# Kernel tuning notes

Hardware: AMD Instinct MI355X
Metric: run time of the kernel (lower is better)

The kernel has to match this reference:

```python
import jax, jax.numpy as jnp
import numpy as np

EPS = 1e-5  # torch GroupNorm default
KNN_K = 16


def _knn_idx(Q, P, K):
    # Q:[B,Nq,3], P:[B,Np,3] -> idx [B,Nq,K], ascending squared distance
    d = (jnp.sum(Q * Q, -1)[:, :, None] + jnp.sum(P * P, -1)[:, None, :]
         - 2.0 * jnp.einsum('bqc,bkc->bqk', Q, P))
    _, idx = jax.lax.top_k(-d, K)
    return idx


def _gather_nbr(feat_bnc, idx_bqk):
    # feat:[B,Np,C], idx:[B,Nq,K] -> [B,Nq,K,C]  (knn_gather)
    return jax.vmap(lambda f, i: f[i])(feat_bnc, idx_bqk)


def _group_norm(x_bcnk, gamma, beta, num_groups=8):
    B, C, N, K = x_bcnk.shape
    G = min(num_groups, C)
    xg = x_bcnk.reshape(B, G, C // G, N, K)
    mu = xg.mean(axis=(2, 3, 4), keepdims=True)
    var = xg.var(axis=(2, 3, 4), keepdims=True)
    xn = ((xg - mu) / jnp.sqrt(var + EPS)).reshape(B, C, N, K)
    return xn * gamma[None, :, None, None] + beta[None, :, None, None]


def _edge_conv(Fq_bcn, Fk_bcn, Pq_b3n, Pk_b3n, k, W, gamma, beta):
    # EdgeConv: concat(x_j - x_i, x_i) -> conv1x1 -> GN -> ReLU -> max over K
    idx = _knn_idx(Pq_b3n.transpose(0, 2, 1), Pk_b3n.transpose(0, 2, 1), k)
    nbr = _gather_nbr(Fk_bcn.transpose(0, 2, 1), idx)          # [B,Nq,K,Cin]
    Fi = jnp.broadcast_to(Fq_bcn.transpose(0, 2, 1)[:, :, None, :], nbr.shape)
    pair = jnp.concatenate([nbr - Fi, Fi], axis=-1)            # [B,Nq,K,2Cin]
    out = jnp.einsum('oc,bnkc->bonk', W, pair)                 # conv 1x1, no bias
    out = _group_norm(out, gamma, beta)
    out = jax.nn.relu(out)
    return out.max(axis=-1)                                    # [B,Cout,Nq]


def _fps_idx(P_b3n, m):
    # Farthest point sampling starting at index 0 (pytorch3d default)
    def one(Pn3):
        d0 = jnp.sum((Pn3 - Pn3[0]) ** 2, -1)
        def step(dists, _):
            nxt = jnp.argmax(dists)
            d = jnp.sum((Pn3 - Pn3[nxt]) ** 2, -1)
            return jnp.minimum(dists, d), nxt
        _, idxs = jax.lax.scan(step, d0, None, length=m - 1)
        return jnp.concatenate([jnp.zeros((1,), jnp.int32), idxs.astype(jnp.int32)])
    return jax.vmap(one)(P_b3n.transpose(0, 2, 1))


def _gather_bcn(x_bcn, idx_bm):
    return jax.vmap(lambda x, i: x[:, i])(x_bcn, idx_bm)


def setup_inputs() -> dict:
    key = jax.random.key(0)
    ks = jax.random.split(key, 8)
    B, N = 2, 8192
    def w(k, shape, s=0.1):
        return jax.random.normal(k, shape, jnp.float32) * s
    return {
        'xyz': jax.random.normal(ks[0], (B, 3, N), jnp.float32),
        'stem_w': w(ks[1], (8, 3)), 'stem_b': jnp.zeros((8,), jnp.float32),
        'w1': w(ks[2], (32, 16)),  'g1': jnp.ones((32,), jnp.float32),  'b1': jnp.zeros((32,), jnp.float32),
        'w2': w(ks[3], (64, 64)),  'g2': jnp.ones((64,), jnp.float32),  'b2': jnp.zeros((64,), jnp.float32),
        'w3': w(ks[4], (64, 128)), 'g3': jnp.ones((64,), jnp.float32),  'b3': jnp.zeros((64,), jnp.float32),
        'w4': w(ks[5], (128, 128)),'g4': jnp.ones((128,), jnp.float32), 'b4': jnp.zeros((128,), jnp.float32),
    }


def reference(xyz, stem_w, stem_b, w1, g1, b1, w2, g2, b2, w3, g3, b3, w4, g4, b4):
    K = KNN_K
    P0 = xyz                                                     # [B,3,N0]
    F0 = jnp.einsum('oc,bcn->bon', stem_w, xyz) + stem_b[None, :, None]
    F0a = _edge_conv(F0, F0, P0, P0, K, w1, g1, b1)              # [B,32,N0]
    N0 = P0.shape[2]
    N1 = max(1, N0 // 4)
    idx1 = _fps_idx(P0, N1)
    P1 = _gather_bcn(P0, idx1)
    F1sk = _gather_bcn(F0a, idx1)
    F1a = _edge_conv(F1sk, F0a, P1, P0, K, w2, g2, b2)           # [B,64,N1]
    N2 = max(1, N1 // 4)
    idx2 = _fps_idx(P1, N2)
    P2 = _gather_bcn(P1, idx2)
    F2sk = _gather_bcn(F1a, idx2)
    F2mid = _edge_conv(F2sk, F1a, P2, P1, K, w3, g3, b3)         # [B,64,N2]
    F2a = _edge_conv(F2mid, F1a, P2, P1, K, w4, g4, b4)          # [B,128,N2]
    return (P0, F0a, P1, F1a, P2, F2a)
```

## Files before the change

kernel.cpp:

```cpp
#include <hip/hip_runtime.h>
#include <math.h>

#define KNN 16

__global__ __launch_bounds__(256) void stem_kernel(const float* __restrict__ xyz,
    const float* __restrict__ w, const float* __restrict__ bias,
    float* __restrict__ F0, int N){
  int id = blockIdx.x*256 + threadIdx.x;
  int n = id % N; int b = id / N;
  float x = xyz[((size_t)b*3+0)*N+n];
  float y = xyz[((size_t)b*3+1)*N+n];
  float z = xyz[((size_t)b*3+2)*N+n];
  #pragma unroll
  for (int o=0;o<8;o++){
    float v = fmaf(w[o*3+0],x, fmaf(w[o*3+1],y, fmaf(w[o*3+2],z, bias[o])));
    F0[((size_t)b*8+o)*N+n] = v;
  }
}

__global__ __launch_bounds__(256) void knn_kernel(
    const float* __restrict__ Pq, const float* __restrict__ Pp,
    float* __restrict__ part_d, int* __restrict__ part_i,
    int Nq, int Np, int CAND){
  __shared__ float4 tile[256];
  int qg = blockIdx.x*256 + threadIdx.x;
  int b  = qg / Nq, qn = qg % Nq;
  int s  = blockIdx.y;
  const float* Pqb = Pq + (size_t)b*3*Nq;
  const float* Ppb = Pp + (size_t)b*3*Np;
  float qx = Pqb[qn], qy = Pqb[Nq+qn], qz = Pqb[2*Nq+qn];
  float qq = __fadd_rn(__fadd_rn(__fmul_rn(qx,qx),__fmul_rn(qy,qy)),__fmul_rn(qz,qz));

  float dl[16]; int il[16];
  #pragma unroll
  for (int u=0;u<16;u++){ dl[u]=INFINITY; il[u]=-1; }
  float maxd = INFINITY; int maxslot = 0;

  int c0 = s*CAND;
  for (int tb=0; tb<CAND; tb+=256){
    int p = c0 + tb + threadIdx.x;
    float px = Ppb[p], py = Ppb[Np+p], pz = Ppb[2*Np+p];
    float pp = __fadd_rn(__fadd_rn(__fmul_rn(px,px),__fmul_rn(py,py)),__fmul_rn(pz,pz));
    __syncthreads();
    tile[threadIdx.x] = make_float4(px,py,pz,pp);
    __syncthreads();
    for (int j=0;j<256;j++){
      float4 c = tile[j];
      float dot = __fadd_rn(__fadd_rn(__fmul_rn(qx,c.x),__fmul_rn(qy,c.y)),__fmul_rn(qz,c.z));
      float dc  = __fsub_rn(__fadd_rn(qq,c.w), __fmul_rn(2.0f,dot));
      if (dc < maxd){
        int pidx = c0 + tb + j;
        #pragma unroll
        for (int u=0;u<16;u++){ bool sel=(maxslot==u); dl[u]=sel?dc:dl[u]; il[u]=sel?pidx:il[u]; }
        maxd = dl[0]; maxslot = 0;
        #pragma unroll
        for (int u=1;u<16;u++){ bool g=(dl[u]>maxd); maxd=g?dl[u]:maxd; maxslot=g?u:maxslot; }
      }
    }
  }
  size_t base = ((size_t)qg*gridDim.y + s)*16;
  #pragma unroll
  for (int u=0;u<16;u++){ part_d[base+u]=dl[u]; part_i[base+u]=il[u]; }
}

__global__ __launch_bounds__(256) void knn_merge(const float* __restrict__ part_d,
    const int* __restrict__ part_i, int* __restrict__ idxk, int S, int total){
  int qg = blockIdx.x*256 + threadIdx.x;
  if (qg >= total) return;
  const float* pd = part_d + (size_t)qg*S*16;
  const int*   pi = part_i + (size_t)qg*S*16;
  float dl[16]; int il[16];
  #pragma unroll
  for (int u=0;u<16;u++){ dl[u]=INFINITY; il[u]=0x7fffffff; }
  float maxd = INFINITY; int maxi = 0x7fffffff; int maxslot = 0;
  int tot = S*16;
  for (int e=0;e<tot;e++){
    float d = pd[e]; int ii = pi[e];
    bool better = (d < maxd) || (d == maxd && ii < maxi);
    if (better){
      #pragma unroll
      for (int u=0;u<16;u++){ bool sel=(maxslot==u); dl[u]=sel?d:dl[u]; il[u]=sel?ii:il[u]; }
      maxd = dl[0]; maxi = il[0]; maxslot = 0;
      #pragma unroll
      for (int u=1;u<16;u++){
        bool g = (dl[u]>maxd) || (dl[u]==maxd && il[u]>maxi);
        maxd=g?dl[u]:maxd; maxi=g?il[u]:maxi; maxslot=g?u:maxslot;
      }
    }
  }
  #pragma unroll
  for (int u=0;u<16;u++) idxk[(size_t)qg*16+u] = il[u];
}

template<int CIN, int COUT>
__global__ __launch_bounds__(1024) void edge_conv_pre(
    const float* __restrict__ Fk, const float* __restrict__ Fi,
    const int* __restrict__ idx, const float* __restrict__ W,
    float* __restrict__ pre, int Nq, int Np){
  constexpr int C2  = 2*CIN;
  constexpr int PAD = C2 + 4;
  constexpr int TO  = (COUT <= 64) ? COUT : 64;
  constexpr int OP  = COUT / TO;
  extern __shared__ float sm[];
  float* Wl = sm;
  float* Pl = sm + COUT*PAD;
  int t = threadIdx.x;
  int n = blockIdx.x, b = blockIdx.y;
  for (int e=t; e<COUT*C2; e += blockDim.x){
    int o=e/C2, c=e%C2; Wl[o*PAD+c] = W[e];
  }
  const int* idxn = idx + ((size_t)b*Nq + n)*16;
  for (int e=t; e<16*C2; e += blockDim.x){
    int k = e/C2, c = e%C2;
    int cc = (c < CIN) ? c : (c-CIN);
    float fi = Fi[((size_t)b*CIN + cc)*Nq + n];
    float v;
    if (c < CIN){ int nb = idxn[k]; v = Fk[((size_t)b*CIN + c)*Np + nb] - fi; }
    else v = fi;
    Pl[k*PAD+c] = v;
  }
  __syncthreads();
  int k = t & 15, o0 = t >> 4;
  #pragma unroll
  for (int op=0; op<OP; op++){
    int o = o0 + op*TO;
    float acc = 0.f;
    #pragma unroll
    for (int c=0;c<C2;c+=4){
      float4 wv = *(const float4*)&Wl[o*PAD+c];
      float4 pv = *(const float4*)&Pl[k*PAD+c];
      acc = fmaf(wv.x,pv.x,acc); acc = fmaf(wv.y,pv.y,acc);
      acc = fmaf(wv.z,pv.z,acc); acc = fmaf(wv.w,pv.w,acc);
    }
    pre[(((size_t)b*COUT + o)*Nq + n)*16 + k] = acc;
  }
}

__global__ __launch_bounds__(256) void gn_reduce(const float* __restrict__ pre,
    double* __restrict__ gsum, int slabLen){
  int b = blockIdx.z, g = blockIdx.y;
  size_t base = ((size_t)(b*8+g))*slabLen;
  int chunkLen = slabLen / gridDim.x;
  const float* p = pre + base + (size_t)blockIdx.x*chunkLen;
  double s=0.0, sq=0.0;
  for (int i = threadIdx.x*4; i < chunkLen; i += 1024){
    float4 v = *(const float4*)(p+i);
    s += (double)v.x; sq = fma((double)v.x,(double)v.x,sq);
    s += (double)v.y; sq = fma((double)v.y,(double)v.y,sq);
    s += (double)v.z; sq = fma((double)v.z,(double)v.z,sq);
    s += (double)v.w; sq = fma((double)v.w,(double)v.w,sq);
  }
  #pragma unroll
  for (int off=32; off>=1; off>>=1){ s += __shfl_down(s, off); sq += __shfl_down(sq, off); }
  __shared__ double ls[4], lq[4];
  int wid = threadIdx.x>>6;
  if ((threadIdx.x&63)==0){ ls[wid]=s; lq[wid]=sq; }
  __syncthreads();
  if (threadIdx.x==0){
    double S=ls[0]+ls[1]+ls[2]+ls[3], Q=lq[0]+lq[1]+lq[2]+lq[3];
    atomicAdd(&gsum[(b*8+g)*2],   S);
    atomicAdd(&gsum[(b*8+g)*2+1], Q);
  }
}

template<int COUT>
__global__ __launch_bounds__(256) void gn_act_max(const float* __restrict__ pre,
    const double* __restrict__ gsum, const float* __restrict__ gamma,
    const float* __restrict__ beta, float* __restrict__ outF, int Nq){
  int id = blockIdx.x*256 + threadIdx.x;
  int o = (id/Nq)%COUT; int b = id/(Nq*COUT);
  int g = o/(COUT/8);
  double s = gsum[(b*8+g)*2], sq = gsum[(b*8+g)*2+1];
  double cnt = (double)(COUT/8)*Nq*16.0;
  double mu  = s/cnt;
  double var = sq/cnt - mu*mu;
  float muf=(float)mu, rstd=(float)(1.0/sqrt(var+1e-5));
  float ga=gamma[o], be=beta[o];
  const float4* p = (const float4*)(pre + (size_t)id*16);
  float m = 0.f;
  #pragma unroll
  for (int q=0;q<4;q++){
    float4 v = p[q];
    m = fmaxf(m, fmaf((v.x-muf)*rstd, ga, be));
    m = fmaxf(m, fmaf((v.y-muf)*rstd, ga, be));
    m = fmaxf(m, fmaf((v.z-muf)*rstd, ga, be));
    m = fmaxf(m, fmaf((v.w-muf)*rstd, ga, be));
  }
  outF[id] = m;
}

template<int CTRL>
__device__ __forceinline__ float dpp_maxf(float x){
  int y = __builtin_amdgcn_update_dpp(0, __float_as_int(x), CTRL, 0xf, 0xf, true);
  return fmaxf(x, __int_as_float(y));
}

template<int PPT, int BLK, int M>
__global__ __launch_bounds__(BLK) void fps_kernel(const float* __restrict__ P,
    int* __restrict__ idx_out){
  constexpr int N  = PPT*BLK;
  constexpr int NW = BLK/64;
  extern __shared__ __align__(16) float sm[];
  float* lx = sm; float* ly = sm+N; float* lz = sm+2*N;
  unsigned long long* wkey = (unsigned long long*)(sm + 3*N);
  int b = blockIdx.x, t = threadIdx.x;
  const float* Pb = P + (size_t)b*3*N;
  float px[PPT], py[PPT], pz[PPT], dist[PPT];
  #pragma unroll
  for (int j=0;j<PPT;j+=4){
    int p = t*PPT + j;
    float4 vx = *(const float4*)&Pb[p];
    float4 vy = *(const float4*)&Pb[N+p];
    float4 vz = *(const float4*)&Pb[2*N+p];
    px[j]=vx.x; px[j+1]=vx.y; px[j+2]=vx.z; px[j+3]=vx.w;
    py[j]=vy.x; py[j+1]=vy.y; py[j+2]=vy.z; py[j+3]=vy.w;
    pz[j]=vz.x; pz[j+1]=vz.y; pz[j+2]=vz.z; pz[j+3]=vz.w;
    #pragma unroll
    for (int u=0;u<4;u++){ lx[p+u]=px[j+u]; ly[p+u]=py[j+u]; lz[p+u]=pz[j+u]; }
  }
  __syncthreads();
  float sx=lx[0], sy=ly[0], sz=lz[0];
  float bd = -1.f; int bj = 0;
  #pragma unroll
  for (int j=0;j<PPT;j++){
    float dx=__fsub_rn(px[j],sx), dy=__fsub_rn(py[j],sy), dz=__fsub_rn(pz[j],sz);
    float dd=__fadd_rn(__fadd_rn(__fmul_rn(dx,dx),__fmul_rn(dy,dy)),__fmul_rn(dz,dz));
    dist[j]=dd;
    bool c = dd > bd; bd = c?dd:bd; bj = c?j:bj;
  }
  int pbest = t*PPT + bj;
  if (t==0) idx_out[(size_t)b*M] = 0;
  int wid = t>>6, lane = t&63;
  int par = 0;
  for (int i=1;i<M;i++){
    float r = bd;
    r = dpp_maxf<0x111>(r);
    r = dpp_maxf<0x112>(r);
    r = dpp_maxf<0x114>(r);
    r = dpp_maxf<0x118>(r);
    r = dpp_maxf<0x142>(r);
    r = dpp_maxf<0x143>(r);
    float wmax = __int_as_float(__builtin_amdgcn_readlane(__float_as_int(r), 63));
    unsigned long long msk = __ballot(bd == wmax);
    int srcl = __ffsll(msk) - 1;
    int wp = __builtin_amdgcn_readlane(pbest, srcl);
    if (lane==0)
      wkey[par*NW + wid] = ((unsigned long long)__float_as_uint(wmax)<<32)
                         | (unsigned)(~(unsigned)wp);
    __syncthreads();
    unsigned long long best = wkey[par*NW];
    #pragma unroll
    for (int w=1;w<NW;w++){ unsigned long long o = wkey[par*NW+w]; best = (o>best)?o:best; }
    unsigned widx = ~(unsigned)best;
    if (t==0) idx_out[(size_t)b*M + i] = (int)widx;
    float nsx = lx[widx], nsy = ly[widx], nsz = lz[widx];
    par ^= 1;
    float nbd = -1.f; int nbj = 0;
    #pragma unroll
    for (int j=0;j<PPT;j++){
      float dx=__fsub_rn(px[j],nsx), dy=__fsub_rn(py[j],nsy), dz=__fsub_rn(pz[j],nsz);
      float dd=__fadd_rn(__fadd_rn(__fmul_rn(dx,dx),__fmul_rn(dy,dy)),__fmul_rn(dz,dz));
      float nd = fminf(dist[j], dd);
      dist[j] = nd;
      bool c = nd > nbd; nbd = c?nd:nbd; nbj = c?j:nbj;
    }
    bd = nbd; pbest = t*PPT + nbj;
  }
}

__global__ __launch_bounds__(256) void gather_kernel(float* __restrict__ dst,
    const float* __restrict__ src, const int* __restrict__ idx,
    int C, int Nsrc, int M){
  int id = blockIdx.x*256 + threadIdx.x;
  int m = id % M; int c = (id/M)%C; int b = id/(M*C);
  dst[id] = src[((size_t)b*C + c)*Nsrc + idx[(size_t)b*M + m]];
}

extern "C" void kernel_launch(void* const* d_in, const int* in_sizes, int n_in,
                              void* d_out, int out_size, void* d_ws, size_t ws_size,
                              hipStream_t stream) {
  const float* xyz    = (const float*)d_in[0];
  const float* stem_w = (const float*)d_in[1];
  const float* stem_b = (const float*)d_in[2];
  const float* w1 = (const float*)d_in[3];
  const float* g1 = (const float*)d_in[4];
  const float* b1 = (const float*)d_in[5];
  const float* w2 = (const float*)d_in[6];
  const float* g2 = (const float*)d_in[7];
  const float* b2 = (const float*)d_in[8];
  const float* w3 = (const float*)d_in[9];
  const float* g3 = (const float*)d_in[10];
  const float* b3 = (const float*)d_in[11];
  const float* w4 = (const float*)d_in[12];
  const float* g4 = (const float*)d_in[13];
  const float* b4 = (const float*)d_in[14];

  float* out = (float*)d_out;
  float* P0o  = out + 0;
  float* F0a  = out + 49152;
  float* P1o  = out + 573440;
  float* F1a  = out + 585728;
  float* P2o  = out + 847872;
  float* F2a  = out + 850944;

  char* ws = (char*)d_ws;
  float* F0     = (float*)(ws + 0);
  float* pre    = (float*)(ws + 524288);
  float* part_d = (float*)(ws + 524288);
  int*   part_i = (int*)  (ws + 524288 + 16777216);
  int*   idxk   = (int*)  (ws + 34078720);
  double* gsum  = (double*)(ws + 35127296);
  int*   idx1   = (int*)  (ws + 35127552);
  int*   idx2   = (int*)  (ws + 35143936);
  float* F1sk   = (float*)(ws + 35148032);
  float* F2sk   = (float*)(ws + 35672320);
  float* F2mid  = (float*)(ws + 35934464);

  size_t smem_c1 = (size_t)(32*20  + 16*20 )*4;
  size_t smem_c2 = (size_t)(64*132 + 16*132)*4;
  size_t smem_c4 = (size_t)(128*132+ 16*132)*4;
  size_t smem_f1 = (size_t)3*8192*4 + 256;
  size_t smem_f2 = (size_t)3*2048*4 + 256;

  hipMemcpyAsync(P0o, xyz, (size_t)49152*4, hipMemcpyDeviceToDevice, stream);
  stem_kernel<<<(2*8192)/256, 256, 0, stream>>>(xyz, stem_w, stem_b, F0, 8192);

  knn_kernel<<<dim3(16384/256, 16), 256, 0, stream>>>(xyz, xyz, part_d, part_i, 8192, 8192, 512);
  knn_merge <<<16384/256, 256, 0, stream>>>(part_d, part_i, idxk, 16, 16384);
  edge_conv_pre<8,32><<<dim3(8192,2), 512, smem_c1, stream>>>(F0, F0, idxk, w1, pre, 8192, 8192);
  hipMemsetAsync(gsum, 0, 256, stream);
  gn_reduce<<<dim3(8,8,2), 256, 0, stream>>>(pre, gsum, 4*8192*16);
  gn_act_max<32><<<(2*32*8192)/256, 256, 0, stream>>>(pre, gsum, g1, b1, F0a, 8192);

  fps_kernel<16,512,2048><<<2, 512, smem_f1, stream>>>(xyz, idx1);
  gather_kernel<<<(2*3*2048)/256, 256, 0, stream>>>(P1o, xyz, idx1, 3, 8192, 2048);
  gather_kernel<<<(2*32*2048)/256, 256, 0, stream>>>(F1sk, F0a, idx1, 32, 8192, 2048);

  knn_kernel<<<dim3(4096/256, 16), 256, 0, stream>>>(P1o, xyz, part_d, part_i, 2048, 8192, 512);
  knn_merge <<<4096/256, 256, 0, stream>>>(part_d, part_i, idxk, 16, 4096);
  edge_conv_pre<32,64><<<dim3(2048,2), 1024, smem_c2, stream>>>(F0a, F1sk, idxk, w2, pre, 2048, 8192);
  hipMemsetAsync(gsum, 0, 256, stream);
  gn_reduce<<<dim3(4,8,2), 256, 0, stream>>>(pre, gsum, 8*2048*16);
  gn_act_max<64><<<(2*64*2048)/256, 256, 0, stream>>>(pre, gsum, g2, b2, F1a, 2048);

  fps_kernel<4,512,512><<<2, 512, smem_f2, stream>>>(P1o, idx2);
  gather_kernel<<<(2*3*512)/256, 256, 0, stream>>>(P2o, P1o, idx2, 3, 2048, 512);
  gather_kernel<<<(2*64*512)/256, 256, 0, stream>>>(F2sk, F1a, idx2, 64, 2048, 512);

  knn_kernel<<<dim3(1024/256, 8), 256, 0, stream>>>(P2o, P1o, part_d, part_i, 512, 2048, 256);
  knn_merge <<<1024/256, 256, 0, stream>>>(part_d, part_i, idxk, 8, 1024);
  edge_conv_pre<64,64><<<dim3(512,2), 1024, smem_c2, stream>>>(F1a, F2sk, idxk, w3, pre, 512, 2048);
  hipMemsetAsync(gsum, 0, 256, stream);
  gn_reduce<<<dim3(1,8,2), 256, 0, stream>>>(pre, gsum, 8*512*16);
  gn_act_max<64><<<(2*64*512)/256, 256, 0, stream>>>(pre, gsum, g3, b3, F2mid, 512);

  edge_conv_pre<64,128><<<dim3(512,2), 1024, smem_c4, stream>>>(F1a, F2mid, idxk, w4, pre, 512, 2048);
  hipMemsetAsync(gsum, 0, 256, stream);
  gn_reduce<<<dim3(2,8,2), 256, 0, stream>>>(pre, gsum, 16*512*16);
  gn_act_max<128><<<(2*128*512)/256, 256, 0, stream>>>(pre, gsum, g4, b4, F2a, 512);

  (void)in_sizes; (void)n_in; (void)out_size; (void)ws_size;
}
```

Baseline: 4.044 ms.

## Morton-sort FPS points with bounding-box pruning and coalesce KNN partial layout

The FPS kernel now bitonic-sorts points by Morton code in shared memory so each thread owns a spatially compact set. It keeps a per-thread bounding box and skips the distance update when the new sample cannot reduce any of its distances. The winning sample's coordinates are broadcast directly, which removes the shared-memory coordinate arrays. KNN partial results are stored row-major over queries so the writes and the merge reads coalesce. The shared-memory size for the CIN=32 edge conv also changes. The pruning uses a fixed quantization grid (offset 8, scale 4) and a 0.999 slack factor, which assume a particular input range. The bitonic sort adds an upfront cost.

```diff
diff --git a/kernel.cpp b/kernel.cpp
--- a/kernel.cpp
+++ b/kernel.cpp
@@ -1,7 +1,7 @@
 #include <hip/hip_runtime.h>
 #include <math.h>
 
-#define KNN 16
+typedef unsigned long long ull;
 
 __global__ __launch_bounds__(256) void stem_kernel(const float* __restrict__ xyz,
     const float* __restrict__ w, const float* __restrict__ bias,
@@ -21,7 +21,7 @@
 __global__ __launch_bounds__(256) void knn_kernel(
     const float* __restrict__ Pq, const float* __restrict__ Pp,
     float* __restrict__ part_d, int* __restrict__ part_i,
-    int Nq, int Np, int CAND){
+    int Nq, int Np, int CAND, int total){
   __shared__ float4 tile[256];
   int qg = blockIdx.x*256 + threadIdx.x;
   int b  = qg / Nq, qn = qg % Nq;
@@ -58,24 +58,25 @@
       }
     }
   }
-  size_t base = ((size_t)qg*gridDim.y + s)*16;
-  #pragma unroll
-  for (int u=0;u<16;u++){ part_d[base+u]=dl[u]; part_i[base+u]=il[u]; }
+  #pragma unroll
+  for (int u=0;u<16;u++){
+    size_t row = (size_t)(s*16+u);
+    part_d[row*total + qg] = dl[u];
+    part_i[row*total + qg] = il[u];
+  }
 }
 
 __global__ __launch_bounds__(256) void knn_merge(const float* __restrict__ part_d,
-    const int* __restrict__ part_i, int* __restrict__ idxk, int S, int total){
+    const int* __restrict__ part_i, int* __restrict__ idxk, int rows, int total){
   int qg = blockIdx.x*256 + threadIdx.x;
   if (qg >= total) return;
-  const float* pd = part_d + (size_t)qg*S*16;
-  const int*   pi = part_i + (size_t)qg*S*16;
   float dl[16]; int il[16];
   #pragma unroll
   for (int u=0;u<16;u++){ dl[u]=INFINITY; il[u]=0x7fffffff; }
   float maxd = INFINITY; int maxi = 0x7fffffff; int maxslot = 0;
-  int tot = S*16;
-  for (int e=0;e<tot;e++){
-    float d = pd[e]; int ii = pi[e];
+  for (int e=0;e<rows;e++){
+    float d = part_d[(size_t)e*total + qg];
+    int  ii = part_i[(size_t)e*total + qg];
     bool better = (d < maxd) || (d == maxd && ii < maxi);
     if (better){
       #pragma unroll
@@ -194,77 +195,129 @@
   int y = __builtin_amdgcn_update_dpp(0, __float_as_int(x), CTRL, 0xf, 0xf, true);
   return fmaxf(x, __int_as_float(y));
 }
+__device__ __forceinline__ unsigned expandb(unsigned v){
+  v &= 0x3FF;
+  v = (v | (v<<16)) & 0x030000FF;
+  v = (v | (v<<8))  & 0x0300F00F;
+  v = (v | (v<<4))  & 0x030C30C3;
+  v = (v | (v<<2))  & 0x09249249;
+  return v;
+}
 
 template<int PPT, int BLK, int M>
 __global__ __launch_bounds__(BLK) void fps_kernel(const float* __restrict__ P,
     int* __restrict__ idx_out){
   constexpr int N  = PPT*BLK;
   constexpr int NW = BLK/64;
-  extern __shared__ __align__(16) float sm[];
-  float* lx = sm; float* ly = sm+N; float* lz = sm+2*N;
-  unsigned long long* wkey = (unsigned long long*)(sm + 3*N);
+  extern __shared__ __align__(16) unsigned smu[];
+  unsigned* keys = smu;
+  ull*     wk    = (ull*)&smu[N];
+  float4*  wc    = (float4*)(wk + 2*NW);
   int b = blockIdx.x, t = threadIdx.x;
   const float* Pb = P + (size_t)b*3*N;
-  float px[PPT], py[PPT], pz[PPT], dist[PPT];
-  #pragma unroll
-  for (int j=0;j<PPT;j+=4){
-    int p = t*PPT + j;
-    float4 vx = *(const float4*)&Pb[p];
-    float4 vy = *(const float4*)&Pb[N+p];
-    float4 vz = *(const float4*)&Pb[2*N+p];
-    px[j]=vx.x; px[j+1]=vx.y; px[j+2]=vx.z; px[j+3]=vx.w;
-    py[j]=vy.x; py[j+1]=vy.y; py[j+2]=vy.z; py[j+3]=vy.w;
-    pz[j]=vz.x; pz[j+1]=vz.y; pz[j+2]=vz.z; pz[j+3]=vz.w;
-    #pragma unroll
-    for (int u=0;u<4;u++){ lx[p+u]=px[j+u]; ly[p+u]=py[j+u]; lz[p+u]=pz[j+u]; }
+
+  for (int i=t; i<N; i+=BLK){
+    float x = Pb[i], y = Pb[N+i], z = Pb[2*N+i];
+    int cx = (int)(__fadd_rn(x,8.f)*4.f); cx = cx<0?0:(cx>63?63:cx);
+    int cy = (int)(__fadd_rn(y,8.f)*4.f); cy = cy<0?0:(cy>63?63:cy);
+    int cz = (int)(__fadd_rn(z,8.f)*4.f); cz = cz<0?0:(cz>63?63:cz);
+    unsigned mo = (expandb(cx)<<2) | (expandb(cy)<<1) | expandb(cz);
+    keys[i] = (mo<<13) | (unsigned)i;
+  }
+  for (unsigned k=2; k<=(unsigned)N; k<<=1){
+    for (unsigned j=k>>1; j>0; j>>=1){
+      __syncthreads();
+      for (int i=t; i<N; i+=BLK){
+        unsigned ixj = (unsigned)i ^ j;
+        if (ixj > (unsigned)i){
+          unsigned a = keys[i], c = keys[ixj];
+          bool up = ((i & k) == 0);
+          if ((a > c) == up){ keys[i]=c; keys[ixj]=a; }
+        }
+      }
+    }
   }
   __syncthreads();
-  float sx=lx[0], sy=ly[0], sz=lz[0];
-  float bd = -1.f; int bj = 0;
+
+  int oidx[PPT]; float px[PPT], py[PPT], pz[PPT], dist[PPT];
+  #pragma unroll
+  for (int j=0;j<PPT;j++){
+    oidx[j] = (int)(keys[t*PPT+j] & 0x1FFF);
+    px[j] = Pb[oidx[j]]; py[j] = Pb[N+oidx[j]]; pz[j] = Pb[2*N+oidx[j]];
+  }
+  float bxmn=px[0],bxmx=px[0],bymn=py[0],bymx=py[0],bzmn=pz[0],bzmx=pz[0];
+  #pragma unroll
+  for (int j=1;j<PPT;j++){
+    bxmn=fminf(bxmn,px[j]); bxmx=fmaxf(bxmx,px[j]);
+    bymn=fminf(bymn,py[j]); bymx=fmaxf(bymx,py[j]);
+    bzmn=fminf(bzmn,pz[j]); bzmx=fmaxf(bzmx,pz[j]);
+  }
+
+  float sx = Pb[0], sy = Pb[N], sz = Pb[2*N];
+  float bd = -1.f; int bi = 0x7fffffff; float bx=0.f, by=0.f, bz=0.f;
   #pragma unroll
   for (int j=0;j<PPT;j++){
     float dx=__fsub_rn(px[j],sx), dy=__fsub_rn(py[j],sy), dz=__fsub_rn(pz[j],sz);
     float dd=__fadd_rn(__fadd_rn(__fmul_rn(dx,dx),__fmul_rn(dy,dy)),__fmul_rn(dz,dz));
     dist[j]=dd;
-    bool c = dd > bd; bd = c?dd:bd; bj = c?j:bj;
-  }
-  int pbest = t*PPT + bj;
+    bool gt = dd > bd, eq = dd == bd;
+    int mn = min(bi, oidx[j]);
+    bd = gt?dd:bd; bx = gt?px[j]:bx; by = gt?py[j]:by; bz = gt?pz[j]:bz;
+    bi = gt?oidx[j]:(eq?mn:bi);
+  }
   if (t==0) idx_out[(size_t)b*M] = 0;
-  int wid = t>>6, lane = t&63;
-  int par = 0;
+
+  int wid = t>>6, lane = t&63, par = 0;
   for (int i=1;i<M;i++){
     float r = bd;
-    r = dpp_maxf<0x111>(r);
-    r = dpp_maxf<0x112>(r);
-    r = dpp_maxf<0x114>(r);
-    r = dpp_maxf<0x118>(r);
-    r = dpp_maxf<0x142>(r);
-    r = dpp_maxf<0x143>(r);
+    r = dpp_maxf<0x111>(r); r = dpp_maxf<0x112>(r);
+    r = dpp_maxf<0x114>(r); r = dpp_maxf<0x118>(r);
+    r = dpp_maxf<0x142>(r); r = dpp_maxf<0x143>(r);
     float wmax = __int_as_float(__builtin_amdgcn_readlane(__float_as_int(r), 63));
-    unsigned long long msk = __ballot(bd == wmax);
-    int srcl = __ffsll(msk) - 1;
-    int wp = __builtin_amdgcn_readlane(pbest, srcl);
-    if (lane==0)
-      wkey[par*NW + wid] = ((unsigned long long)__float_as_uint(wmax)<<32)
-                         | (unsigned)(~(unsigned)wp);
+    ull msk = __ballot(bd == wmax);
+    int bestl = __ffsll(msk) - 1;
+    int wbi = __builtin_amdgcn_readlane(bi, bestl);
+    ull rest = msk & (msk-1);
+    if (rest){
+      while (rest){
+        int l = __ffsll(rest)-1; rest &= rest-1;
+        int c = __builtin_amdgcn_readlane(bi, l);
+        if (c < wbi){ wbi = c; bestl = l; }
+      }
+    }
+    float wx = __int_as_float(__builtin_amdgcn_readlane(__float_as_int(bx), bestl));
+    float wy = __int_as_float(__builtin_amdgcn_readlane(__float_as_int(by), bestl));
+    float wz = __int_as_float(__builtin_amdgcn_readlane(__float_as_int(bz), bestl));
+    if (lane==0){
+      wk[par*NW+wid] = ((ull)__float_as_uint(wmax)<<32) | (unsigned)(~(unsigned)wbi);
+      wc[par*NW+wid] = make_float4(wx,wy,wz,0.f);
+    }
     __syncthreads();
-    unsigned long long best = wkey[par*NW];
+    ull best = wk[par*NW]; int bw = 0;
     #pragma unroll
-    for (int w=1;w<NW;w++){ unsigned long long o = wkey[par*NW+w]; best = (o>best)?o:best; }
-    unsigned widx = ~(unsigned)best;
-    if (t==0) idx_out[(size_t)b*M + i] = (int)widx;
-    float nsx = lx[widx], nsy = ly[widx], nsz = lz[widx];
+    for (int w=1;w<NW;w++){ ull o = wk[par*NW+w]; if (o > best){ best=o; bw=w; } }
+    float4 sc = wc[par*NW+bw];
+    if (t==0) idx_out[(size_t)b*M + i] = (int)(~(unsigned)best);
     par ^= 1;
-    float nbd = -1.f; int nbj = 0;
-    #pragma unroll
-    for (int j=0;j<PPT;j++){
-      float dx=__fsub_rn(px[j],nsx), dy=__fsub_rn(py[j],nsy), dz=__fsub_rn(pz[j],nsz);
-      float dd=__fadd_rn(__fadd_rn(__fmul_rn(dx,dx),__fmul_rn(dy,dy)),__fmul_rn(dz,dz));
-      float nd = fminf(dist[j], dd);
-      dist[j] = nd;
-      bool c = nd > nbd; nbd = c?nd:nbd; nbj = c?j:nbj;
-    }
-    bd = nbd; pbest = t*PPT + nbj;
+    float ex = fmaxf(fmaxf(__fsub_rn(bxmn,sc.x), __fsub_rn(sc.x,bxmx)), 0.f);
+    float ey = fmaxf(fmaxf(__fsub_rn(bymn,sc.y), __fsub_rn(sc.y,bymx)), 0.f);
+    float ez = fmaxf(fmaxf(__fsub_rn(bzmn,sc.z), __fsub_rn(sc.z,bzmx)), 0.f);
+    float lb = ex*ex + ey*ey + ez*ez;
+    if (!(lb*0.999f > bd)){
+      float nbd = -1.f; int nbi = 0x7fffffff; float nbx=0.f, nby=0.f, nbz=0.f;
+      #pragma unroll
+      for (int j=0;j<PPT;j++){
+        float dx=__fsub_rn(px[j],sc.x), dy=__fsub_rn(py[j],sc.y), dz=__fsub_rn(pz[j],sc.z);
+        float dd=__fadd_rn(__fadd_rn(__fmul_rn(dx,dx),__fmul_rn(dy,dy)),__fmul_rn(dz,dz));
+        float nd = fminf(dist[j], dd);
+        dist[j] = nd;
+        bool gt = nd > nbd, eq = nd == nbd;
+        int mn = min(nbi, oidx[j]);
+        nbd = gt?nd:nbd; nbx = gt?px[j]:nbx; nby = gt?py[j]:nby; nbz = gt?pz[j]:nbz;
+        nbi = gt?oidx[j]:(eq?mn:nbi);
+      }
+      bd=nbd; bi=nbi; bx=nbx; by=nby; bz=nbz;
+    }
   }
 }
 
@@ -317,16 +370,17 @@
   float* F2mid  = (float*)(ws + 35934464);
 
   size_t smem_c1 = (size_t)(32*20  + 16*20 )*4;
-  size_t smem_c2 = (size_t)(64*132 + 16*132)*4;
+  size_t smem_c2 = (size_t)(64*68  + 16*68 )*4;
+  size_t smem_c3 = (size_t)(64*132 + 16*132)*4;
   size_t smem_c4 = (size_t)(128*132+ 16*132)*4;
-  size_t smem_f1 = (size_t)3*8192*4 + 256;
-  size_t smem_f2 = (size_t)3*2048*4 + 256;
+  size_t smem_f1 = (size_t)8192*4 + 512;
+  size_t smem_f2 = (size_t)2048*4 + 512;
 
   hipMemcpyAsync(P0o, xyz, (size_t)49152*4, hipMemcpyDeviceToDevice, stream);
   stem_kernel<<<(2*8192)/256, 256, 0, stream>>>(xyz, stem_w, stem_b, F0, 8192);
 
-  knn_kernel<<<dim3(16384/256, 16), 256, 0, stream>>>(xyz, xyz, part_d, part_i, 8192, 8192, 512);
-  knn_merge <<<16384/256, 256, 0, stream>>>(part_d, part_i, idxk, 16, 16384);
+  knn_kernel<<<dim3(16384/256, 16), 256, 0, stream>>>(xyz, xyz, part_d, part_i, 8192, 8192, 512, 16384);
+  knn_merge <<<16384/256, 256, 0, stream>>>(part_d, part_i, idxk, 256, 16384);
   edge_conv_pre<8,32><<<dim3(8192,2), 512, smem_c1, stream>>>(F0, F0, idxk, w1, pre, 8192, 8192);
   hipMemsetAsync(gsum, 0, 256, stream);
   gn_reduce<<<dim3(8,8,2), 256, 0, stream>>>(pre, gsum, 4*8192*16);
@@ -336,8 +390,8 @@
   gather_kernel<<<(2*3*2048)/256, 256, 0, stream>>>(P1o, xyz, idx1, 3, 8192, 2048);
   gather_kernel<<<(2*32*2048)/256, 256, 0, stream>>>(F1sk, F0a, idx1, 32, 8192, 2048);
 
-  knn_kernel<<<dim3(4096/256, 16), 256, 0, stream>>>(P1o, xyz, part_d, part_i, 2048, 8192, 512);
-  knn_merge <<<4096/256, 256, 0, stream>>>(part_d, part_i, idxk, 16, 4096);
+  knn_kernel<<<dim3(4096/256, 16), 256, 0, stream>>>(P1o, xyz, part_d, part_i, 2048, 8192, 512, 4096);
+  knn_merge <<<4096/256, 256, 0, stream>>>(part_d, part_i, idxk, 256, 4096);
   edge_conv_pre<32,64><<<dim3(2048,2), 1024, smem_c2, stream>>>(F0a, F1sk, idxk, w2, pre, 2048, 8192);
   hipMemsetAsync(gsum, 0, 256, stream);
   gn_reduce<<<dim3(4,8,2), 256, 0, stream>>>(pre, gsum, 8*2048*16);
@@ -347,9 +401,9 @@
   gather_kernel<<<(2*3*512)/256, 256, 0, stream>>>(P2o, P1o, idx2, 3, 2048, 512);
   gather_kernel<<<(2*64*512)/256, 256, 0, stream>>>(F2sk, F1a, idx2, 64, 2048, 512);
 
-  knn_kernel<<<dim3(1024/256, 8), 256, 0, stream>>>(P2o, P1o, part_d, part_i, 512, 2048, 256);
-  knn_merge <<<1024/256, 256, 0, stream>>>(part_d, part_i, idxk, 8, 1024);
-  edge_conv_pre<64,64><<<dim3(512,2), 1024, smem_c2, stream>>>(F1a, F2sk, idxk, w3, pre, 512, 2048);
+  knn_kernel<<<dim3(1024/256, 8), 256, 0, stream>>>(P2o, P1o, part_d, part_i, 512, 2048, 256, 1024);
+  knn_merge <<<1024/256, 256, 0, stream>>>(part_d, part_i, idxk, 128, 1024);
+  edge_conv_pre<64,64><<<dim3(512,2), 1024, smem_c3, stream>>>(F1a, F2sk, idxk, w3, pre, 512, 2048);
   hipMemsetAsync(gsum, 0, 256, stream);
   gn_reduce<<<dim3(1,8,2), 256, 0, stream>>>(pre, gsum, 8*512*16);
   gn_act_max<64><<<(2*64*512)/256, 256, 0, stream>>>(pre, gsum, g3, b3, F2mid, 512);
```

New measurement: 4.656 ms. 15.1% more time.
